# Optimization experiments

Hardware: AMD Instinct MI355X
Metric: run time of the kernel (lower is better)

## Reference

```python
import jax, jax.numpy as jnp
import numpy as np

WEIGHT = 1.0  # init kwarg
B, N, M, D = 32, 128, 128, 256


def _hungarian(cost):
    """O(n^3) Hungarian (Jonker-Volgenant potentials form) on host numpy.
    cost: [n, m] with n <= m. Returns col index assigned to each row
    (row_ind is implicitly arange(n), matching scipy.linear_sum_assignment).
    """
    cost = np.asarray(cost, dtype=np.float64)
    n, m = cost.shape
    u = np.zeros(n + 1)
    v = np.zeros(m + 1)
    p = np.zeros(m + 1, dtype=np.int64)   # p[j] = row (1-based) matched to col j
    way = np.zeros(m + 1, dtype=np.int64)
    for i in range(1, n + 1):
        p[0] = i
        j0 = 0
        minv = np.full(m + 1, np.inf)
        used = np.zeros(m + 1, dtype=bool)
        while True:
            used[j0] = True
            i0 = p[j0]
            free = ~used[1:]
            cur = cost[i0 - 1, :] - u[i0] - v[1:]
            upd = free & (cur < minv[1:])
            minv[1:][upd] = cur[upd]
            way[1:][upd] = j0
            masked = np.where(free, minv[1:], np.inf)
            j1 = int(np.argmin(masked)) + 1
            delta = masked[j1 - 1]
            u[p[used]] += delta
            v[used] -= delta
            minv[1:][free] -= delta
            j0 = j1
            if p[j0] == 0:
                break
        while j0:
            j1 = way[j0]
            p[j0] = p[j1]
            j0 = j1
    col_of_row = np.zeros(n, dtype=np.int64)
    for j in range(1, m + 1):
        if p[j] > 0:
            col_of_row[p[j] - 1] = j - 1
    return col_of_row


def _pairwise_mse(p, g):
    """cost[b,i,j] = mean_d (p[b,i,d]-g[b,j,d])^2, fused without [B,N,M,D] tensor."""
    d = p.shape[-1]
    p2 = jnp.sum(p * p, axis=-1)                    # [B,N]
    g2 = jnp.sum(g * g, axis=-1)                    # [B,M]
    pg = jnp.einsum('bnd,bmd->bnm', p, g)           # [B,N,M]
    return (p2[:, :, None] + g2[:, None, :] - 2.0 * pg) / d


def setup_inputs() -> dict:
    key = jax.random.key(0)
    k1, k2 = jax.random.split(key)
    batch_prediction = jax.random.normal(k1, (B, N, D), dtype=jnp.float32)
    batch_groundtruth = jax.random.normal(k2, (B, M, D), dtype=jnp.float32)
    return {"batch_prediction": batch_prediction,
            "batch_groundtruth": batch_groundtruth}


def reference(batch_prediction, batch_groundtruth):
    b, n = batch_prediction.shape[0], batch_prediction.shape[1]
    cost = _pairwise_mse(batch_prediction, batch_groundtruth)   # [B,N,M]
    cost_np = np.asarray(jax.device_get(cost))
    # Hungarian assignment on host (matches scipy.linear_sum_assignment; CPU-bound)
    cols = jnp.asarray(np.stack([_hungarian(cost_np[bi]) for bi in range(b)]))  # [B,N]
    matched = cost[jnp.arange(b)[:, None], jnp.arange(n)[None, :], cols]        # [B,N]
    loss = matched.mean(axis=1).sum() / b * WEIGHT
    return jnp.reshape(loss, (1,))
```

## Files before the change

kernel.cpp:

```cpp
#include <hip/hip_runtime.h>
#include <float.h>

#define Bc 32
#define Nn 128
#define Dd 256

template <int CTRL>
__device__ __forceinline__ float dpp_addsrc(float x) {
    return __int_as_float(__builtin_amdgcn_update_dpp(0, __float_as_int(x), CTRL,
                                                      0xf, 0xf, false));
}
__device__ __forceinline__ float wave_sum_lane63(float x) {
    x += dpp_addsrc<0x121>(x);
    x += dpp_addsrc<0x122>(x);
    x += dpp_addsrc<0x124>(x);
    x += dpp_addsrc<0x128>(x);
    x += dpp_addsrc<0x142>(x);
    x += dpp_addsrc<0x143>(x);
    return x;
}

template <int CTRL>
__device__ __forceinline__ unsigned dpp_movu(unsigned x) {
    return (unsigned)__builtin_amdgcn_update_dpp((int)0xFFFFFFFFu, (int)x, CTRL,
                                                 0xf, 0xf, false);
}
__device__ __forceinline__ unsigned wave_umin_lane63(unsigned x) {
    x = min(x, dpp_movu<0x121>(x));
    x = min(x, dpp_movu<0x122>(x));
    x = min(x, dpp_movu<0x124>(x));
    x = min(x, dpp_movu<0x128>(x));
    x = min(x, dpp_movu<0x142>(x));
    x = min(x, dpp_movu<0x143>(x));
    return x;
}

template <int CTRL>
__device__ __forceinline__ float dpp_movf(float x) {
    return __int_as_float(__builtin_amdgcn_update_dpp(0x7f7fffff, __float_as_int(x),
                                                      CTRL, 0xf, 0xf, false));
}
template <int CTRL>
__device__ __forceinline__ void dpp2min_step(float& m1, float& m2) {
    float o1 = dpp_movf<CTRL>(m1);
    float o2 = dpp_movf<CTRL>(m2);
    float n1 = fminf(m1, o1);
    m2 = fminf(fmaxf(m1, o1), fminf(m2, o2));
    m1 = n1;
}

__device__ __forceinline__ float readlane_f(float v, int lane) {
    return __int_as_float(__builtin_amdgcn_readlane(__float_as_int(v), lane));
}

__global__ __launch_bounds__(64) void cost_kernel(const float* __restrict__ P,
                                                  const float* __restrict__ G,
                                                  float* __restrict__ C,
                                                  float* __restrict__ out) {
    const int b = blockIdx.y;
    const int i = blockIdx.x;
    const int t = threadIdx.x;

    if (b == 0 && i == 0 && t == 0) *out = 0.0f;

    const float4 pv = ((const float4*)(P + ((size_t)b * Nn + i) * Dd))[t];
    const float4* g4 = (const float4*)(G + (size_t)b * Nn * Dd);
    float* crow = C + ((size_t)b * Nn + i) * Nn;

    for (int j = 0; j < Nn; j += 2) {
        float4 gv0 = g4[(size_t)j * 64 + t];
        float4 gv1 = g4[(size_t)(j + 1) * 64 + t];
        float dx0 = pv.x - gv0.x, dy0 = pv.y - gv0.y, dz0 = pv.z - gv0.z, dw0 = pv.w - gv0.w;
        float dx1 = pv.x - gv1.x, dy1 = pv.y - gv1.y, dz1 = pv.z - gv1.z, dw1 = pv.w - gv1.w;
        float s0 = dx0 * dx0 + dy0 * dy0 + dz0 * dz0 + dw0 * dw0;
        float s1 = dx1 * dx1 + dy1 * dy1 + dz1 * dz1 + dw1 * dw1;
        s0 = wave_sum_lane63(s0);
        s1 = wave_sum_lane63(s1);
        if (t == 63) {
            crow[j]     = s0 * (1.0f / (float)Dd);
            crow[j + 1] = s1 * (1.0f / (float)Dd);
        }
    }
}

__global__ __launch_bounds__(64) void hungarian_kernel(const float* __restrict__ Call,
                                                       float* __restrict__ out) {
    const int b = blockIdx.x;
    const int t = threadIdx.x;

    __shared__ float Csh[Nn * Nn];
    __shared__ int claim[Nn];

    {
        const float4* src = (const float4*)(Call + (size_t)b * Nn * Nn);
        float4* dst = (float4*)Csh;
#pragma unroll
        for (int k = 0; k < (Nn * Nn / 4) / 64; ++k)
            dst[k * 64 + t] = src[k * 64 + t];
    }
    claim[t] = 0x7fffffff;
    claim[t + 64] = 0x7fffffff;
    __syncthreads();

    float bestA = FLT_MAX, bestB = FLT_MAX;
    int argA = 0, argB = 0;
    for (int i = 0; i < Nn; ++i) {
        float c0 = Csh[i * Nn + t];
        float c1 = Csh[i * Nn + t + 64];
        if (c0 < bestA) { bestA = c0; argA = i; }
        if (c1 < bestB) { bestB = c1; argB = i; }
    }
    float vA = bestA, vB = bestB;
    atomicMin(&claim[argA], t);
    atomicMin(&claim[argB], t + 64);
    __syncthreads();

    float uA = 0.0f, uB = 0.0f;
    float wA = 0.0f, wB = 0.0f;
    int pA = 0, pB = 0;
    if (claim[argA] == t)      pA = argA + 1;
    if (claim[argB] == t + 64) pB = argB + 1;

    unsigned long long fmA = __ballot(claim[t] == 0x7fffffff);
    unsigned long long fmB = __ballot(claim[t + 64] == 0x7fffffff);

    for (int pass = 0; pass < 2; ++pass) {
        if (!(fmA | fmB)) break;
        unsigned long long remA = fmA, remB = fmB;
        int guard = 0;
        while ((remA | remB) != 0ull && guard++ < 256) {
            int l, i, slotR;
            if (remA) { l = __ffsll(remA) - 1; remA &= remA - 1; i = l + 1;  slotR = 0;
                        if (!((fmA >> l) & 1)) continue; }
            else      { l = __ffsll(remB) - 1; remB &= remB - 1; i = l + 65; slotR = 1;
                        if (!((fmB >> l) & 1)) continue; }

            const float* crow = &Csh[(i - 1) * Nn];
            float cur0 = crow[t] - vA;
            float cur1 = crow[t + 64] - vB;
            float m1 = fminf(cur0, cur1);
            float m2 = fmaxf(cur0, cur1);
            dpp2min_step<0x121>(m1, m2);
            dpp2min_step<0x122>(m1, m2);
            dpp2min_step<0x124>(m1, m2);
            dpp2min_step<0x128>(m1, m2);
            dpp2min_step<0x142>(m1, m2);
            dpp2min_step<0x143>(m1, m2);
            float s_m1 = readlane_f(m1, 63);
            float s_m2 = readlane_f(m2, 63);

            unsigned long long b0 = __ballot(cur0 == s_m1);
            unsigned long long b1 = __ballot(cur1 == s_m1);
            int j1 = b0 ? __ffsll(b0) : (__ffsll(b1) + 64);
            int lane1 = (j1 - 1) & 63, slot1 = (j1 - 1) >> 6;

            if (t == l) { if (slotR == 0) uA = s_m2; else uB = s_m2; }

            int k0 = __builtin_amdgcn_readlane(slot1 ? pB : pA, lane1);
            bool strict = (s_m1 < s_m2);
            if (!strict && k0 != 0) continue;

            if (t == lane1) {
                if (slot1 == 0) { vA += s_m1 - s_m2; pA = i; wA = s_m2; }
                else            { vB += s_m1 - s_m2; pB = i; wB = s_m2; }
            }
            if (slotR == 0) fmA &= ~(1ull << l); else fmB &= ~(1ull << l);
            if (k0 != 0) {
                int kl = (k0 - 1) & 63;
                if (k0 <= 64) { fmA |= 1ull << kl; remA |= 1ull << kl; }
                else          { fmB |= 1ull << kl; remB |= 1ull << kl; }
            }
        }
    }

    for (int slotR = 0; slotR < 2; ++slotR) {
        unsigned long long mask = slotR ? fmB : fmA;
        while (mask) {
            int l = __ffsll(mask) - 1;
            mask &= mask - 1;
            int i = l + 1 + slotR * 64;

            float minvA = FLT_MAX, minvB = FLT_MAX;
            int wayA = 0, wayB = 0;
            bool usedA = false, usedB = false;
            bool rUA = false, rUB = false;
            if (t == l) { if (slotR == 0) rUA = true; else rUB = true; }

            int s_j0 = 0;
            float s_u = readlane_f(slotR ? uB : uA, l);
            int s_j1;

            float c0 = Csh[(i - 1) * Nn + t];
            float c1 = Csh[(i - 1) * Nn + t + 64];

            for (;;) {
                if (!usedA) {
                    float cur = fmaxf(c0 - s_u - vA, 0.0f);
                    if (cur < minvA) { minvA = cur; wayA = s_j0; }
                }
                if (!usedB) {
                    float cur = fmaxf(c1 - s_u - vB, 0.0f);
                    if (cur < minvB) { minvB = cur; wayB = s_j0; }
                }

                unsigned kA = (__float_as_uint(usedA ? FLT_MAX : minvA) & 0xFFFFFF00u)
                              | (unsigned)t;
                unsigned kB = (__float_as_uint(usedB ? FLT_MAX : minvB) & 0xFFFFFF00u)
                              | (unsigned)(t + 64);
                unsigned k = wave_umin_lane63(min(kA, kB));
                unsigned s_key = (unsigned)__builtin_amdgcn_readlane((int)k, 63);
                float s_delta = __uint_as_float(s_key & 0xFFFFFF00u);
                s_j1 = (int)(s_key & 0xFFu) + 1;

                int lane1 = (s_j1 - 1) & 63;
                int slot1 = (s_j1 - 1) >> 6;
                int s_p = __builtin_amdgcn_readlane(slot1 ? pB : pA, lane1);
                float s_w = readlane_f(slot1 ? wB : wA, lane1);

                int nrow = (s_p > 0 ? s_p : 1) - 1;
                float nc0 = Csh[nrow * Nn + t];
                float nc1 = Csh[nrow * Nn + t + 64];

                if (usedA) { vA -= s_delta; wA += s_delta; }
                else       { minvA = fmaxf(minvA - s_delta, 0.0f); }
                if (usedB) { vB -= s_delta; wB += s_delta; }
                else       { minvB = fmaxf(minvB - s_delta, 0.0f); }
                if (rUA) uA += s_delta;
                if (rUB) uB += s_delta;

                if (s_p == 0) break;

                if (t == lane1) { if (slot1 == 0) usedA = true; else usedB = true; }
                {
                    int r = s_p - 1;
                    if (t == (r & 63)) { if ((r >> 6) == 0) rUA = true; else rUB = true; }
                }
                s_j0 = s_j1;
                s_u = s_w;
                c0 = nc0;
                c1 = nc1;
            }

            int s_j = s_j1;
            while (s_j) {
                int lane = (s_j - 1) & 63;
                int slot = (s_j - 1) >> 6;
                int s_jprev = __builtin_amdgcn_readlane(slot ? wayB : wayA, lane);
                int s_pnew;
                if (s_jprev == 0) {
                    s_pnew = i;
                } else {
                    int lp = (s_jprev - 1) & 63;
                    int sp = (s_jprev - 1) >> 6;
                    s_pnew = __builtin_amdgcn_readlane(sp ? pB : pA, lp);
                }
                int rl = (s_pnew - 1) & 63;
                int rs = (s_pnew - 1) >> 6;
                float s_unew = readlane_f(rs ? uB : uA, rl);
                if (t == lane) {
                    if (slot == 0) { pA = s_pnew; wA = s_unew; }
                    else           { pB = s_pnew; wB = s_unew; }
                }
                s_j = s_jprev;
            }
        }
    }

    float tot = Csh[(pA - 1) * Nn + t] + Csh[(pB - 1) * Nn + t + 64];
    tot = wave_sum_lane63(tot);

    if (t == 63) {
        atomicAdd(out, tot * (1.0f / ((float)Nn * (float)Bc)));
    }
}

extern "C" void kernel_launch(void* const* d_in, const int* in_sizes, int n_in,
                              void* d_out, int out_size, void* d_ws, size_t ws_size,
                              hipStream_t stream) {
    const float* P = (const float*)d_in[0];
    const float* G = (const float*)d_in[1];
    float* out = (float*)d_out;
    float* C = (float*)d_ws;

    dim3 gcost(Nn, Bc);
    cost_kernel<<<gcost, 64, 0, stream>>>(P, G, C, out);
    hungarian_kernel<<<Bc, 64, 0, stream>>>(C, out);
}
```

Baseline: 549.2 us.

## Interleave cost row layout for float2 LDS reads and branchless Hungarian inner loop

The cost kernel now writes each row interleaved so that columns t and t+64 sit next to each other, which lets the Hungarian kernel fetch both with one float2 LDS load. The augmenting-path inner loop is made branchless: used columns are masked through large sentinel values instead of conditionals. The row owner p is read with a single packed readlane rather than selecting between two registers. This aims to cut LDS instructions and cross-lane reads on the serial critical path, at the cost of relying on sentinel arithmetic and on p values fitting in 8 bits.

```diff
diff --git a/kernel.cpp b/kernel.cpp
--- a/kernel.cpp
+++ b/kernel.cpp
@@ -4,6 +4,8 @@
 #define Bc 32
 #define Nn 128
 #define Dd 256
+
+#define BIGV 1e37f
 
 template <int CTRL>
 __device__ __forceinline__ float dpp_addsrc(float x) {
@@ -77,8 +79,9 @@
         s0 = wave_sum_lane63(s0);
         s1 = wave_sum_lane63(s1);
         if (t == 63) {
-            crow[j]     = s0 * (1.0f / (float)Dd);
-            crow[j + 1] = s1 * (1.0f / (float)Dd);
+            int base = (j < 64) ? (2 * j) : (2 * (j - 64) + 1);
+            crow[base]     = s0 * (1.0f / (float)Dd);
+            crow[base + 2] = s1 * (1.0f / (float)Dd);
         }
     }
 }
@@ -102,13 +105,15 @@
     claim[t + 64] = 0x7fffffff;
     __syncthreads();
 
+    const float2* C2 = (const float2*)Csh;
+
     float bestA = FLT_MAX, bestB = FLT_MAX;
     int argA = 0, argB = 0;
+#pragma unroll 8
     for (int i = 0; i < Nn; ++i) {
-        float c0 = Csh[i * Nn + t];
-        float c1 = Csh[i * Nn + t + 64];
-        if (c0 < bestA) { bestA = c0; argA = i; }
-        if (c1 < bestB) { bestB = c1; argB = i; }
+        float2 c = C2[i * 64 + t];
+        if (c.x < bestA) { bestA = c.x; argA = i; }
+        if (c.y < bestB) { bestB = c.y; argB = i; }
     }
     float vA = bestA, vB = bestB;
     atomicMin(&claim[argA], t);
@@ -135,9 +140,9 @@
             else      { l = __ffsll(remB) - 1; remB &= remB - 1; i = l + 65; slotR = 1;
                         if (!((fmB >> l) & 1)) continue; }
 
-            const float* crow = &Csh[(i - 1) * Nn];
-            float cur0 = crow[t] - vA;
-            float cur1 = crow[t + 64] - vB;
+            float2 cc = C2[(i - 1) * 64 + t];
+            float cur0 = cc.x - vA;
+            float cur1 = cc.y - vB;
             float m1 = fminf(cur0, cur1);
             float m2 = fmaxf(cur0, cur1);
             dpp2min_step<0x121>(m1, m2);
@@ -180,65 +185,77 @@
             mask &= mask - 1;
             int i = l + 1 + slotR * 64;
 
+            int pPk = (pA & 0xFF) | ((pB & 0xFF) << 8);
+
             float minvA = FLT_MAX, minvB = FLT_MAX;
             int wayA = 0, wayB = 0;
             bool usedA = false, usedB = false;
-            bool rUA = false, rUB = false;
-            if (t == l) { if (slotR == 0) rUA = true; else rUB = true; }
+            bool rUA = (slotR == 0) && (t == l);
+            bool rUB = (slotR == 1) && (t == l);
 
             int s_j0 = 0;
             float s_u = readlane_f(slotR ? uB : uA, l);
             int s_j1;
 
-            float c0 = Csh[(i - 1) * Nn + t];
-            float c1 = Csh[(i - 1) * Nn + t + 64];
+            float bA = vA + s_u;
+            float bB = vB + s_u;
+
+            float2 c = C2[(i - 1) * 64 + t];
 
             for (;;) {
-                if (!usedA) {
-                    float cur = fmaxf(c0 - s_u - vA, 0.0f);
-                    if (cur < minvA) { minvA = cur; wayA = s_j0; }
-                }
-                if (!usedB) {
-                    float cur = fmaxf(c1 - s_u - vB, 0.0f);
-                    if (cur < minvB) { minvB = cur; wayB = s_j0; }
-                }
-
-                unsigned kA = (__float_as_uint(usedA ? FLT_MAX : minvA) & 0xFFFFFF00u)
-                              | (unsigned)t;
-                unsigned kB = (__float_as_uint(usedB ? FLT_MAX : minvB) & 0xFFFFFF00u)
-                              | (unsigned)(t + 64);
+                float cur0 = fmaxf(c.x - bA, 0.0f);
+                float cur1 = fmaxf(c.y - bB, 0.0f);
+                bool u0 = (cur0 < minvA) && !usedA;
+                bool u1 = (cur1 < minvB) && !usedB;
+                wayA = u0 ? s_j0 : wayA;
+                wayB = u1 ? s_j0 : wayB;
+                minvA = fminf(minvA, cur0);
+                minvB = fminf(minvB, cur1);
+
+                unsigned kA = (__float_as_uint(minvA) & 0xFFFFFF00u) | (unsigned)t;
+                unsigned kB = (__float_as_uint(minvB) & 0xFFFFFF00u) | (unsigned)(t + 64);
                 unsigned k = wave_umin_lane63(min(kA, kB));
                 unsigned s_key = (unsigned)__builtin_amdgcn_readlane((int)k, 63);
+
+                int s_col = (int)(s_key & 0xFFu);
+                s_j1 = s_col + 1;
                 float s_delta = __uint_as_float(s_key & 0xFFFFFF00u);
-                s_j1 = (int)(s_key & 0xFFu) + 1;
-
-                int lane1 = (s_j1 - 1) & 63;
-                int slot1 = (s_j1 - 1) >> 6;
-                int s_p = __builtin_amdgcn_readlane(slot1 ? pB : pA, lane1);
-                float s_w = readlane_f(slot1 ? wB : wA, lane1);
-
+
+                int s_pp = __builtin_amdgcn_readlane(pPk, s_col & 63);
+                int s_p = (s_pp >> ((s_col >> 6) << 3)) & 0xFF;
                 int nrow = (s_p > 0 ? s_p : 1) - 1;
-                float nc0 = Csh[nrow * Nn + t];
-                float nc1 = Csh[nrow * Nn + t + 64];
-
-                if (usedA) { vA -= s_delta; wA += s_delta; }
-                else       { minvA = fmaxf(minvA - s_delta, 0.0f); }
-                if (usedB) { vB -= s_delta; wB += s_delta; }
-                else       { minvB = fmaxf(minvB - s_delta, 0.0f); }
-                if (rUA) uA += s_delta;
-                if (rUB) uB += s_delta;
+                float2 nc = C2[nrow * 64 + t];
+
+                float s_wA = readlane_f(wA, s_col & 63);
+                float s_wB = readlane_f(wB, s_col & 63);
+                float s_w = (s_col >> 6) ? s_wB : s_wA;
+
+                vA -= usedA ? s_delta : 0.0f;
+                wA += usedA ? s_delta : 0.0f;
+                vB -= usedB ? s_delta : 0.0f;
+                wB += usedB ? s_delta : 0.0f;
+                uA += rUA ? s_delta : 0.0f;
+                uB += rUB ? s_delta : 0.0f;
+                minvA = fmaxf(minvA - s_delta, 0.0f);
+                minvB = fmaxf(minvB - s_delta, 0.0f);
 
                 if (s_p == 0) break;
 
-                if (t == lane1) { if (slot1 == 0) usedA = true; else usedB = true; }
-                {
-                    int r = s_p - 1;
-                    if (t == (r & 63)) { if ((r >> 6) == 0) rUA = true; else rUB = true; }
-                }
+                bool mk0 = (s_col == t);
+                bool mk1 = (s_col == t + 64);
+                usedA = usedA || mk0;
+                usedB = usedB || mk1;
+                minvA = mk0 ? BIGV : minvA;
+                minvB = mk1 ? BIGV : minvB;
+                int r = s_p - 1;
+                rUA = rUA || (r == t);
+                rUB = rUB || (r == t + 64);
+
                 s_j0 = s_j1;
                 s_u = s_w;
-                c0 = nc0;
-                c1 = nc1;
+                bA = (usedA ? -BIGV : vA) + s_u;
+                bB = (usedB ? -BIGV : vB) + s_u;
+                c = nc;
             }
 
             int s_j = s_j1;
@@ -266,7 +283,7 @@
         }
     }
 
-    float tot = Csh[(pA - 1) * Nn + t] + Csh[(pB - 1) * Nn + t + 64];
+    float tot = Csh[(pA - 1) * Nn + 2 * t] + Csh[(pB - 1) * Nn + 2 * t + 1];
     tot = wave_sum_lane63(tot);
 
     if (t == 63) {
```

After: 564.9 us. 1.03x slower.

## Add column-reduction style potential tightening pass before augmenting path search

Applied to the files above, without the earlier changes.

Inserts a pass over all rows that, for every row that claimed a column during the initial greedy step, computes the minimum reduced cost over all other columns and lowers that column's potential by that amount (a JV-style reduction transfer). Tighter dual potentials are meant to make the later augmenting-path searches for unmatched rows shorter. The cost is an extra serial loop of 128 wave-wide min reductions.

```diff
diff --git a/kernel.cpp b/kernel.cpp
--- a/kernel.cpp
+++ b/kernel.cpp
@@ -124,6 +124,39 @@
     unsigned long long fmA = __ballot(claim[t] == 0x7fffffff);
     unsigned long long fmB = __ballot(claim[t + 64] == 0x7fffffff);
 
+    {
+        int rcA = claim[t];
+        int rcB = claim[t + 64];
+        float c0 = Csh[t];
+        float c1 = Csh[t + 64];
+        for (int r = 0; r < Nn; ++r) {
+            int s_c = __builtin_amdgcn_readlane((r & 64) ? rcB : rcA, r & 63);
+            int pr = (r + 1) & (Nn - 1);
+            float n0 = Csh[pr * Nn + t];
+            float n1 = Csh[pr * Nn + t + 64];
+            if (s_c != 0x7fffffff) {
+                bool ex0 = (t == s_c);
+                bool ex1 = (t + 64 == s_c);
+                float cur0 = ex0 ? FLT_MAX : (c0 - vA);
+                float cur1 = ex1 ? FLT_MAX : (c1 - vB);
+                float m = fminf(cur0, cur1);
+                m = fminf(m, dpp_movf<0x121>(m));
+                m = fminf(m, dpp_movf<0x122>(m));
+                m = fminf(m, dpp_movf<0x124>(m));
+                m = fminf(m, dpp_movf<0x128>(m));
+                m = fminf(m, dpp_movf<0x142>(m));
+                m = fminf(m, dpp_movf<0x143>(m));
+                float mu = readlane_f(m, 63);
+                if (ex0) { vA -= mu; wA = mu; }
+                if (ex1) { vB -= mu; wB = mu; }
+                if (t == (r & 63)) {
+                    if (r < 64) uA = mu; else uB = mu;
+                }
+            }
+            c0 = n0; c1 = n1;
+        }
+    }
+
     for (int pass = 0; pass < 2; ++pass) {
         if (!(fmA | fmB)) break;
         unsigned long long remA = fmA, remB = fmB;
```

Result: faster. 534.6 us (-2.7%).
